# Optimization experiments

Hardware: AMD Instinct MI355X
Metric: run time of the kernel (lower is better)

The kernel has to match this reference:

```python
import jax, jax.numpy as jnp
import numpy as np

B, NL2, NRC, NIN = 32768, 4, 8, 41
NCTRL = NIN + NL2 + NIN  # 86


def _blur(n):
    # tridiagonal blur: 0.8 on diag, 0.1 on the two off-diagonals (symmetric)
    return 0.8 * jnp.eye(n, dtype=jnp.float32) \
         + 0.1 * jnp.eye(n, k=1, dtype=jnp.float32) \
         + 0.1 * jnp.eye(n, k=-1, dtype=jnp.float32)


def _leaky(x):
    return jnp.where(x >= 0, x, 0.2 * x)  # LeakyReLU(0.2)


def _passgate(w, b, rc, x):
    # w: [B,out,in,rc] clamped to [-1,1]; rc: [B,rc]; x: [B,in] -> [B,out]
    w2 = jnp.einsum('boir,br->boi', jnp.clip(w, -1.0, 1.0), rc)
    return jnp.einsum('boi,bi->bo', w2, x) + b


def setup_inputs() -> dict:
    key = jax.random.key(0)
    ks = jax.random.split(key, 4)
    s_f = np.float32(np.sqrt(2.0 / (NIN * NRC)))
    s_r = np.float32(np.sqrt(2.0 / (NL2 * NRC)))
    inp = jax.random.normal(ks[0], (B, NIN), dtype=jnp.float32)
    fpg_w = jnp.clip(jax.random.normal(ks[1], (B, NL2, NIN, NRC), dtype=jnp.float32) * s_f, -1.0, 1.0)
    rpg_w = jnp.clip(jax.random.normal(ks[2], (B, NIN, NL2, NRC), dtype=jnp.float32) * s_r, -1.0, 1.0)
    fpg_b = jnp.zeros((B, NL2), dtype=jnp.float32)
    rpg_b = jnp.zeros((B, NIN), dtype=jnp.float32)
    # pgctrl: shared nn.Linear(86, 8) (default torch init ~ U(-1/sqrt(86), 1/sqrt(86)))
    bound = np.float32(1.0 / np.sqrt(NCTRL))
    kw, kb = jax.random.split(ks[3])
    pgctrl_w = jax.random.uniform(kw, (NRC, NCTRL), dtype=jnp.float32, minval=-bound, maxval=bound)
    pgctrl_b = jax.random.uniform(kb, (NRC,), dtype=jnp.float32, minval=-bound, maxval=bound)
    return {"inp": inp, "fpg_w": fpg_w, "fpg_b": fpg_b,
            "rpg_w": rpg_w, "rpg_b": rpg_b,
            "pgctrl_w": pgctrl_w, "pgctrl_b": pgctrl_b}


def reference(inp, fpg_w, fpg_b, rpg_w, rpg_b, pgctrl_w, pgctrl_b):
    rcblur = _blur(NRC)   # [8,8]
    l2blur = _blur(NL2)   # [4,4]
    # initial state buffers are zeros; note l2old/rcold are NOT updated inside
    # the outer loop (faithful to the original), only l1i carries over.
    l2old = jnp.zeros((B, NL2), dtype=inp.dtype)
    rcold = jnp.zeros((B, NRC), dtype=inp.dtype)
    l1i = jnp.zeros((B, NIN), dtype=inp.dtype)
    l2 = l2old
    rc = rcold
    for _ in range(2):
        rcin = jnp.concatenate([inp, l2old, inp - l1i], axis=1)  # [B,86]
        rc = _leaky(rcin @ pgctrl_w.T + pgctrl_b)
        rc = jnp.clip(0.4 * rc + 0.6 * rcold, -0.2, 1.0)
        for _ in range(3):
            rc = rc @ rcblur.T
        l2 = _passgate(fpg_w, fpg_b, rc, inp) * 0.1 + 0.9 * l2old
        l2 = jnp.clip(l2, -0.2, 1.0)
        for _ in range(2):
            l2 = l2 @ l2blur.T
        l1i = jnp.clip(_passgate(rpg_w, rpg_b, rc, l2), -0.2, 1.0)
    return (l1i, l2, rc)
```

## Files before the change

kernel.cpp:

```cpp
#include <hip/hip_runtime.h>

#define B_ROWS 32768
#define NIN 41
#define NL2 4
#define NRC 8

__device__ __forceinline__ float clampf(float v, float lo, float hi) {
    return fminf(fmaxf(v, lo), hi);
}

__device__ __forceinline__ float4 clamp4(float4 v) {
    v.x = clampf(v.x, -1.f, 1.f);
    v.y = clampf(v.y, -1.f, 1.f);
    v.z = clampf(v.z, -1.f, 1.f);
    v.w = clampf(v.w, -1.f, 1.f);
    return v;
}

__device__ __forceinline__ float wave_sum(float v) {
    #pragma unroll
    for (int m = 1; m < 64; m <<= 1)
        v += __shfl_xor(v, m, 64);
    return v;
}

__global__ void __launch_bounds__(256) pgnet_kernel(
    const float* __restrict__ inp,
    const float* __restrict__ fpg_w,
    const float* __restrict__ fpg_b,
    const float* __restrict__ rpg_w,
    const float* __restrict__ rpg_b,
    const float* __restrict__ pgw,
    const float* __restrict__ pgb,
    float* __restrict__ out)
{
    const int lane = threadIdx.x & 63;
    const int row  = blockIdx.x * 4 + (threadIdx.x >> 6);
    const bool act = lane < NIN;
    const int  i   = lane;

    const float x = act ? inp[row * NIN + i] : 0.0f;

    float4 fw[NL2][2];
    {
        const float* fb_ = fpg_w + (size_t)row * 1312;
        #pragma unroll
        for (int o = 0; o < NL2; ++o) {
            if (act) {
                fw[o][0] = clamp4(*(const float4*)(fb_ + o * 328 + i * 8));
                fw[o][1] = clamp4(*(const float4*)(fb_ + o * 328 + i * 8 + 4));
            } else {
                fw[o][0] = make_float4(0.f, 0.f, 0.f, 0.f);
                fw[o][1] = make_float4(0.f, 0.f, 0.f, 0.f);
            }
        }
    }

    float4 rw[8];
    {
        const float* rb_ = rpg_w + (size_t)row * 1312 + (size_t)i * 32;
        #pragma unroll
        for (int j = 0; j < 8; ++j)
            rw[j] = act ? clamp4(((const float4*)rb_)[j]) : make_float4(0.f, 0.f, 0.f, 0.f);
    }

    float W2[NRC];
    float A[NRC];
    #pragma unroll
    for (int r = 0; r < NRC; ++r) {
        const float w1 = act ? pgw[r * 86 + i] : 0.f;
        const float w2 = act ? pgw[r * 86 + 45 + i] : 0.f;
        W2[r] = w2;
        A[r]  = wave_sum(x * (w1 + w2)) + pgb[r];
    }

    float fb[NL2];
    #pragma unroll
    for (int o = 0; o < NL2; ++o) fb[o] = fpg_b[row * NL2 + o];
    const float rb = act ? rpg_b[row * NIN + i] : 0.f;

    float l1 = 0.0f;
    float rc[NRC];
    float l2[NL2];

    #pragma unroll
    for (int it = 0; it < 2; ++it) {
        #pragma unroll
        for (int r = 0; r < NRC; ++r) {
            const float corr = wave_sum(l1 * W2[r]);
            float v = A[r] - corr;
            v = (v >= 0.f) ? v : 0.2f * v;
            rc[r] = clampf(0.4f * v, -0.2f, 1.0f);
        }
        #pragma unroll
        for (int t = 0; t < 3; ++t) {
            float tmp[NRC];
            #pragma unroll
            for (int r = 0; r < NRC; ++r) {
                float v = 0.8f * rc[r];
                if (r > 0)        v += 0.1f * rc[r - 1];
                if (r < NRC - 1)  v += 0.1f * rc[r + 1];
                tmp[r] = v;
            }
            #pragma unroll
            for (int r = 0; r < NRC; ++r) rc[r] = tmp[r];
        }
        #pragma unroll
        for (int o = 0; o < NL2; ++o) {
            const float d = fw[o][0].x * rc[0] + fw[o][0].y * rc[1]
                          + fw[o][0].z * rc[2] + fw[o][0].w * rc[3]
                          + fw[o][1].x * rc[4] + fw[o][1].y * rc[5]
                          + fw[o][1].z * rc[6] + fw[o][1].w * rc[7];
            const float s = wave_sum(x * d) + fb[o];
            l2[o] = clampf(0.1f * s, -0.2f, 1.0f);
        }
        #pragma unroll
        for (int t = 0; t < 2; ++t) {
            float tmp[NL2];
            #pragma unroll
            for (int o = 0; o < NL2; ++o) {
                float v = 0.8f * l2[o];
                if (o > 0)        v += 0.1f * l2[o - 1];
                if (o < NL2 - 1)  v += 0.1f * l2[o + 1];
                tmp[o] = v;
            }
            #pragma unroll
            for (int o = 0; o < NL2; ++o) l2[o] = tmp[o];
        }
        float acc = rb;
        #pragma unroll
        for (int o = 0; o < NL2; ++o) {
            const float d = rw[2 * o].x * rc[0] + rw[2 * o].y * rc[1]
                          + rw[2 * o].z * rc[2] + rw[2 * o].w * rc[3]
                          + rw[2 * o + 1].x * rc[4] + rw[2 * o + 1].y * rc[5]
                          + rw[2 * o + 1].z * rc[6] + rw[2 * o + 1].w * rc[7];
            acc += l2[o] * d;
        }
        l1 = clampf(acc, -0.2f, 1.0f);
    }

    if (act) out[(size_t)row * NIN + i] = l1;
    if (lane < NL2) {
        float v = l2[0];
        #pragma unroll
        for (int o = 1; o < NL2; ++o) if (lane == o) v = l2[o];
        out[(size_t)B_ROWS * NIN + (size_t)row * NL2 + lane] = v;
    }
    if (lane < NRC) {
        float v = rc[0];
        #pragma unroll
        for (int r = 1; r < NRC; ++r) if (lane == r) v = rc[r];
        out[(size_t)B_ROWS * (NIN + NL2) + (size_t)row * NRC + lane] = v;
    }
}

extern "C" void kernel_launch(void* const* d_in, const int* in_sizes, int n_in,
                              void* d_out, int out_size, void* d_ws, size_t ws_size,
                              hipStream_t stream) {
    const float* inp   = (const float*)d_in[0];
    const float* fpg_w = (const float*)d_in[1];
    const float* fpg_b = (const float*)d_in[2];
    const float* rpg_w = (const float*)d_in[3];
    const float* rpg_b = (const float*)d_in[4];
    const float* pgw   = (const float*)d_in[5];
    const float* pgb   = (const float*)d_in[6];
    float* out = (float*)d_out;

    dim3 grid(B_ROWS / 4);
    dim3 block(256);
    hipLaunchKernelGGL(pgnet_kernel, grid, block, 0, stream,
                       inp, fpg_w, fpg_b, rpg_w, rpg_b, pgw, pgb, out);
}
```

Baseline: 419.6 us.

## Precompute x·fpg_w contractions, use DPP wave reductions, skip zero first-iteration correction

Replaces the shuffle-based wave sum with a DPP row-shift/broadcast reduction that reads the total from lane 63. The forward passgate is reordered so that the 32 contractions of x with each fpg_w column are reduced once before the loop, leaving each iteration with a per-row 8-term dot product instead of wave reductions. The l1 correction reduction is skipped on the first iteration, where l1 is zero. This cuts the per-iteration cross-lane work but adds 32 up-front reductions, and the kernel is probably bound by weight loads.

```diff
diff --git a/kernel.cpp b/kernel.cpp
--- a/kernel.cpp
+++ b/kernel.cpp
@@ -9,19 +9,26 @@
     return fminf(fmaxf(v, lo), hi);
 }
 
-__device__ __forceinline__ float4 clamp4(float4 v) {
-    v.x = clampf(v.x, -1.f, 1.f);
-    v.y = clampf(v.y, -1.f, 1.f);
-    v.z = clampf(v.z, -1.f, 1.f);
-    v.w = clampf(v.w, -1.f, 1.f);
-    return v;
+__device__ __forceinline__ float clamp1(float v) {
+    return fminf(fmaxf(v, -1.f), 1.f);
 }
 
-__device__ __forceinline__ float wave_sum(float v) {
-    #pragma unroll
-    for (int m = 1; m < 64; m <<= 1)
-        v += __shfl_xor(v, m, 64);
-    return v;
+template <int Ctrl>
+__device__ __forceinline__ int dpp_add(int x) {
+    return __float_as_int(
+        __int_as_float(x) +
+        __int_as_float(__builtin_amdgcn_update_dpp(0, x, Ctrl, 0xf, 0xf, true)));
+}
+
+__device__ __forceinline__ float wave_sum_uniform(float v) {
+    int x = __float_as_int(v);
+    x = dpp_add<0x111>(x);
+    x = dpp_add<0x112>(x);
+    x = dpp_add<0x114>(x);
+    x = dpp_add<0x118>(x);
+    x = dpp_add<0x142>(x);
+    x = dpp_add<0x143>(x);
+    return __int_as_float(__builtin_amdgcn_readlane(x, 63));
 }
 
 __global__ void __launch_bounds__(256) pgnet_kernel(
@@ -37,119 +44,126 @@
     const int lane = threadIdx.x & 63;
     const int row  = blockIdx.x * 4 + (threadIdx.x >> 6);
     const bool act = lane < NIN;
-    const int  i   = lane;
 
-    const float x = act ? inp[row * NIN + i] : 0.0f;
+    const float x = act ? inp[row * NIN + lane] : 0.0f;
 
-    float4 fw[NL2][2];
+    float fw[NL2][NRC];
     {
-        const float* fb_ = fpg_w + (size_t)row * 1312;
+        const float* fp = fpg_w + (size_t)row * 1312 + (size_t)lane * 8;
         #pragma unroll
         for (int o = 0; o < NL2; ++o) {
-            if (act) {
-                fw[o][0] = clamp4(*(const float4*)(fb_ + o * 328 + i * 8));
-                fw[o][1] = clamp4(*(const float4*)(fb_ + o * 328 + i * 8 + 4));
-            } else {
-                fw[o][0] = make_float4(0.f, 0.f, 0.f, 0.f);
-                fw[o][1] = make_float4(0.f, 0.f, 0.f, 0.f);
-            }
+            float4 t0 = act ? *(const float4*)(fp + o * 328)     : make_float4(0,0,0,0);
+            float4 t1 = act ? *(const float4*)(fp + o * 328 + 4) : make_float4(0,0,0,0);
+            fw[o][0] = clamp1(t0.x); fw[o][1] = clamp1(t0.y);
+            fw[o][2] = clamp1(t0.z); fw[o][3] = clamp1(t0.w);
+            fw[o][4] = clamp1(t1.x); fw[o][5] = clamp1(t1.y);
+            fw[o][6] = clamp1(t1.z); fw[o][7] = clamp1(t1.w);
         }
     }
 
-    float4 rw[8];
+    float rw[NL2][NRC];
     {
-        const float* rb_ = rpg_w + (size_t)row * 1312 + (size_t)i * 32;
+        const float* rp = rpg_w + (size_t)row * 1312 + (size_t)lane * 32;
         #pragma unroll
-        for (int j = 0; j < 8; ++j)
-            rw[j] = act ? clamp4(((const float4*)rb_)[j]) : make_float4(0.f, 0.f, 0.f, 0.f);
+        for (int o = 0; o < NL2; ++o) {
+            float4 t0 = act ? ((const float4*)rp)[2 * o]     : make_float4(0,0,0,0);
+            float4 t1 = act ? ((const float4*)rp)[2 * o + 1] : make_float4(0,0,0,0);
+            rw[o][0] = clamp1(t0.x); rw[o][1] = clamp1(t0.y);
+            rw[o][2] = clamp1(t0.z); rw[o][3] = clamp1(t0.w);
+            rw[o][4] = clamp1(t1.x); rw[o][5] = clamp1(t1.y);
+            rw[o][6] = clamp1(t1.z); rw[o][7] = clamp1(t1.w);
+        }
     }
 
     float W2[NRC];
     float A[NRC];
     #pragma unroll
     for (int r = 0; r < NRC; ++r) {
-        const float w1 = act ? pgw[r * 86 + i] : 0.f;
-        const float w2 = act ? pgw[r * 86 + 45 + i] : 0.f;
+        const float w1 = act ? pgw[r * 86 + lane]      : 0.f;
+        const float w2 = act ? pgw[r * 86 + 45 + lane] : 0.f;
         W2[r] = w2;
-        A[r]  = wave_sum(x * (w1 + w2)) + pgb[r];
+        A[r]  = wave_sum_uniform(x * (w1 + w2)) + pgb[r];
     }
+
+    float F[NL2][NRC];
+    #pragma unroll
+    for (int o = 0; o < NL2; ++o)
+        #pragma unroll
+        for (int r = 0; r < NRC; ++r)
+            F[o][r] = wave_sum_uniform(x * fw[o][r]);
 
     float fb[NL2];
     #pragma unroll
     for (int o = 0; o < NL2; ++o) fb[o] = fpg_b[row * NL2 + o];
-    const float rb = act ? rpg_b[row * NIN + i] : 0.f;
+    const float rb = act ? rpg_b[row * NIN + lane] : 0.f;
 
     float l1 = 0.0f;
-    float rc[NRC];
-    float l2[NL2];
+    float rcv[NRC], l2v[NL2];
 
     #pragma unroll
     for (int it = 0; it < 2; ++it) {
         #pragma unroll
         for (int r = 0; r < NRC; ++r) {
-            const float corr = wave_sum(l1 * W2[r]);
-            float v = A[r] - corr;
-            v = (v >= 0.f) ? v : 0.2f * v;
-            rc[r] = clampf(0.4f * v, -0.2f, 1.0f);
+            float pre = A[r];
+            if (it > 0) pre -= wave_sum_uniform(l1 * W2[r]);
+            float v = (pre >= 0.f) ? pre : 0.2f * pre;
+            rcv[r] = clampf(0.4f * v, -0.2f, 1.0f);
         }
         #pragma unroll
         for (int t = 0; t < 3; ++t) {
             float tmp[NRC];
             #pragma unroll
             for (int r = 0; r < NRC; ++r) {
-                float v = 0.8f * rc[r];
-                if (r > 0)        v += 0.1f * rc[r - 1];
-                if (r < NRC - 1)  v += 0.1f * rc[r + 1];
+                float v = 0.8f * rcv[r];
+                if (r > 0)       v += 0.1f * rcv[r - 1];
+                if (r < NRC - 1) v += 0.1f * rcv[r + 1];
                 tmp[r] = v;
             }
             #pragma unroll
-            for (int r = 0; r < NRC; ++r) rc[r] = tmp[r];
+            for (int r = 0; r < NRC; ++r) rcv[r] = tmp[r];
         }
         #pragma unroll
         for (int o = 0; o < NL2; ++o) {
-            const float d = fw[o][0].x * rc[0] + fw[o][0].y * rc[1]
-                          + fw[o][0].z * rc[2] + fw[o][0].w * rc[3]
-                          + fw[o][1].x * rc[4] + fw[o][1].y * rc[5]
-                          + fw[o][1].z * rc[6] + fw[o][1].w * rc[7];
-            const float s = wave_sum(x * d) + fb[o];
-            l2[o] = clampf(0.1f * s, -0.2f, 1.0f);
+            float s = fb[o];
+            #pragma unroll
+            for (int r = 0; r < NRC; ++r) s += F[o][r] * rcv[r];
+            l2v[o] = clampf(0.1f * s, -0.2f, 1.0f);
         }
         #pragma unroll
         for (int t = 0; t < 2; ++t) {
             float tmp[NL2];
             #pragma unroll
             for (int o = 0; o < NL2; ++o) {
-                float v = 0.8f * l2[o];
-                if (o > 0)        v += 0.1f * l2[o - 1];
-                if (o < NL2 - 1)  v += 0.1f * l2[o + 1];
+                float v = 0.8f * l2v[o];
+                if (o > 0)       v += 0.1f * l2v[o - 1];
+                if (o < NL2 - 1) v += 0.1f * l2v[o + 1];
                 tmp[o] = v;
             }
             #pragma unroll
-            for (int o = 0; o < NL2; ++o) l2[o] = tmp[o];
+            for (int o = 0; o < NL2; ++o) l2v[o] = tmp[o];
         }
         float acc = rb;
         #pragma unroll
         for (int o = 0; o < NL2; ++o) {
-            const float d = rw[2 * o].x * rc[0] + rw[2 * o].y * rc[1]
-                          + rw[2 * o].z * rc[2] + rw[2 * o].w * rc[3]
-                          + rw[2 * o + 1].x * rc[4] + rw[2 * o + 1].y * rc[5]
-                          + rw[2 * o + 1].z * rc[6] + rw[2 * o + 1].w * rc[7];
-            acc += l2[o] * d;
+            float d = 0.f;
+            #pragma unroll
+            for (int r = 0; r < NRC; ++r) d += rw[o][r] * rcv[r];
+            acc += l2v[o] * d;
         }
         l1 = clampf(acc, -0.2f, 1.0f);
     }
 
-    if (act) out[(size_t)row * NIN + i] = l1;
+    if (act) out[(size_t)row * NIN + lane] = l1;
     if (lane < NL2) {
-        float v = l2[0];
+        float v = l2v[0];
         #pragma unroll
-        for (int o = 1; o < NL2; ++o) if (lane == o) v = l2[o];
+        for (int o = 1; o < NL2; ++o) if (lane == o) v = l2v[o];
         out[(size_t)B_ROWS * NIN + (size_t)row * NL2 + lane] = v;
     }
     if (lane < NRC) {
-        float v = rc[0];
+        float v = rcv[0];
         #pragma unroll
-        for (int r = 1; r < NRC; ++r) if (lane == r) v = rc[r];
+        for (int r = 1; r < NRC; ++r) if (lane == r) v = rcv[r];
         out[(size_t)B_ROWS * (NIN + NL2) + (size_t)row * NRC + lane] = v;
     }
 }
```

Result: faster. 401.7 us (-4.3%).
